# Kernel tuning notes

Hardware: AMD Instinct MI355X
Metric: run time of the kernel (lower is better)

## Reference

```python
import jax, jax.numpy as jnp
import numpy as np

N_QUBITS = 14  # matches init kwarg; state_size = 2**14 = 16384
BATCH = 4096

def setup_inputs() -> dict:
    key = jax.random.key(0)
    phi = jax.random.normal(key, (BATCH, 2 ** N_QUBITS), dtype=jnp.float32)
    return {"phi": phi}

def _fwht(x):
    """Fast Walsh-Hadamard transform, identical butterfly order to had_big:
    view as [B, 2, 2, ..., 2] and for each qubit axis i replace (a, b) with
    (a+b, a-b), then scale by 2**(-n/2)."""
    B, N = x.shape
    n = int(round(np.log2(N)))
    for i in range(n):
        # axis i of the [2]*n view == axis 2 of this reshape
        x = x.reshape(B, 2 ** i, 2, N // (2 ** (i + 1)))
        a = x[:, :, 0, :]
        b = x[:, :, 1, :]
        x = jnp.stack([a + b, a - b], axis=2)
    return x.reshape(B, N) * jnp.asarray(2.0 ** (-n / 2.0), dtype=x.dtype)

def reference(phi):
    return _fwht(phi)
```

## Files before the change

### kernel.cpp

```cpp
#include <hip/hip_runtime.h>


#define NF4 4096
#define SCALE 0.0078125f

__device__ __forceinline__ int swz(int F) { return F ^ ((F >> 3) & 7); }

__device__ __forceinline__ void bfly2(float4& a, float4& b) {
    float ax = a.x, ay = a.y, az = a.z, aw = a.w;
    float bx = b.x, by = b.y, bz = b.z, bw = b.w;
    a.x = ax + bx; a.y = ay + by; a.z = az + bz; a.w = aw + bw;
    b.x = ax - bx; b.y = ay - by; b.z = az - bz; b.w = aw - bw;
}

__device__ __forceinline__ void bfly8(float4 v[8]) {
    bfly2(v[0], v[1]); bfly2(v[2], v[3]); bfly2(v[4], v[5]); bfly2(v[6], v[7]);
    bfly2(v[0], v[2]); bfly2(v[1], v[3]); bfly2(v[4], v[6]); bfly2(v[5], v[7]);
    bfly2(v[0], v[4]); bfly2(v[1], v[5]); bfly2(v[2], v[6]); bfly2(v[3], v[7]);
}

__device__ __forceinline__ void bfly_inner(float4& t) {
    float a = t.x + t.y, b = t.x - t.y;
    float c = t.z + t.w, d = t.z - t.w;
    t.x = a + c; t.y = b + d; t.z = a - c; t.w = b - d;
}

__global__ __launch_bounds__(512)
void fwht_kernel(const float* __restrict__ in, float* __restrict__ out) {
    __shared__ float4 lds[NF4];

    const int row  = blockIdx.x;
    const int tid  = threadIdx.x;
    const int lane = tid & 63;
    const int w    = tid >> 6;

    const float4* in4  = (const float4*)in  + (size_t)row * NF4;
    float4*       out4 = (float4*)out       + (size_t)row * NF4;

    float4 v[8];

#pragma unroll
    for (int j = 0; j < 8; ++j) v[j] = in4[tid + 512 * j];
#pragma unroll
    for (int j = 0; j < 8; ++j) bfly_inner(v[j]);
    bfly8(v);

#pragma unroll
    for (int j = 0; j < 8; ++j) lds[swz(tid + 512 * j)] = v[j];
    __syncthreads();

    {
        const int base = 8 * lane + 512 * w;
#pragma unroll
        for (int g = 0; g < 8; ++g) v[g] = lds[swz(base + g)];
        bfly8(v);
#pragma unroll
        for (int g = 0; g < 8; ++g) lds[swz(base + g)] = v[g];
    }
    __syncthreads();

    {
        const int base = (tid & 7) + 64 * ((tid >> 3) & 7) + 512 * w;
#pragma unroll
        for (int g = 0; g < 8; ++g) v[g] = lds[swz(base + 8 * g)];
        bfly8(v);
#pragma unroll
        for (int g = 0; g < 8; ++g) lds[swz(base + 8 * g)] = v[g];
    }
    __syncthreads();

    {
        const int base = lane + 512 * w;
#pragma unroll
        for (int g = 0; g < 8; ++g) v[g] = lds[swz(base + 64 * g)];
        bfly8(v);
#pragma unroll
        for (int g = 0; g < 8; ++g) {
            float4 t = v[g];
            t.x *= SCALE; t.y *= SCALE; t.z *= SCALE; t.w *= SCALE;
            out4[base + 64 * g] = t;
        }
    }
}

extern "C" void kernel_launch(void* const* d_in, const int* in_sizes, int n_in,
                              void* d_out, int out_size, void* d_ws, size_t ws_size,
                              hipStream_t stream) {
    const float* phi = (const float*)d_in[0];
    float* out = (float*)d_out;
    fwht_kernel<<<4096, 512, 0, stream>>>(phi, out);
}
```

Before: 430.6 us.

## Drop intra-wave barriers, use nontemporal global I/O, simplify swizzle indexing

After the first block barrier, each wavefront works only on its own 512-element slice of LDS, so the two later __syncthreads are removed. Global loads and stores become nontemporal builtins to avoid cache pollution on the streaming read/write. The XOR swizzle is folded into precomputed per-thread offsets and the butterflies use native vector types to cut address and ALU overhead. Dropping the barriers is only correct if the 64-wide wavefront assumption and in-order LDS access within a wave hold.

```diff
diff --git a/kernel.cpp b/kernel.cpp
--- a/kernel.cpp
+++ b/kernel.cpp
@@ -4,22 +4,21 @@
 #define NF4 4096
 #define SCALE 0.0078125f
 
-__device__ __forceinline__ int swz(int F) { return F ^ ((F >> 3) & 7); }
+typedef float f4 __attribute__((ext_vector_type(4)));
 
-__device__ __forceinline__ void bfly2(float4& a, float4& b) {
-    float ax = a.x, ay = a.y, az = a.z, aw = a.w;
-    float bx = b.x, by = b.y, bz = b.z, bw = b.w;
-    a.x = ax + bx; a.y = ay + by; a.z = az + bz; a.w = aw + bw;
-    b.x = ax - bx; b.y = ay - by; b.z = az - bz; b.w = aw - bw;
+__device__ __forceinline__ void bfly2(f4& a, f4& b) {
+    f4 t = a;
+    a = t + b;
+    b = t - b;
 }
 
-__device__ __forceinline__ void bfly8(float4 v[8]) {
+__device__ __forceinline__ void bfly8(f4 v[8]) {
     bfly2(v[0], v[1]); bfly2(v[2], v[3]); bfly2(v[4], v[5]); bfly2(v[6], v[7]);
     bfly2(v[0], v[2]); bfly2(v[1], v[3]); bfly2(v[4], v[6]); bfly2(v[5], v[7]);
     bfly2(v[0], v[4]); bfly2(v[1], v[5]); bfly2(v[2], v[6]); bfly2(v[3], v[7]);
 }
 
-__device__ __forceinline__ void bfly_inner(float4& t) {
+__device__ __forceinline__ void bfly_inner(f4& t) {
     float a = t.x + t.y, b = t.x - t.y;
     float c = t.z + t.w, d = t.z - t.w;
     t.x = a + c; t.y = b + d; t.z = a - c; t.w = b - d;
@@ -27,59 +26,59 @@
 
 __global__ __launch_bounds__(512)
 void fwht_kernel(const float* __restrict__ in, float* __restrict__ out) {
-    __shared__ float4 lds[NF4];
+    __shared__ f4 lds[NF4];
 
-    const int row  = blockIdx.x;
     const int tid  = threadIdx.x;
     const int lane = tid & 63;
     const int w    = tid >> 6;
 
-    const float4* in4  = (const float4*)in  + (size_t)row * NF4;
-    float4*       out4 = (float4*)out       + (size_t)row * NF4;
+    const f4* in4  = (const f4*)in  + (size_t)blockIdx.x * NF4;
+    f4*       out4 = (f4*)out       + (size_t)blockIdx.x * NF4;
 
-    float4 v[8];
+    f4 v[8];
 
 #pragma unroll
-    for (int j = 0; j < 8; ++j) v[j] = in4[tid + 512 * j];
+    for (int j = 0; j < 8; ++j)
+        v[j] = __builtin_nontemporal_load(in4 + tid + 512 * j);
 #pragma unroll
     for (int j = 0; j < 8; ++j) bfly_inner(v[j]);
     bfly8(v);
 
+    const int st = tid ^ ((tid >> 3) & 7);
 #pragma unroll
-    for (int j = 0; j < 8; ++j) lds[swz(tid + 512 * j)] = v[j];
+    for (int j = 0; j < 8; ++j) lds[st + 512 * j] = v[j];
     __syncthreads();
 
     {
+        const int s    = lane & 7;
         const int base = 8 * lane + 512 * w;
 #pragma unroll
-        for (int g = 0; g < 8; ++g) v[g] = lds[swz(base + g)];
+        for (int g = 0; g < 8; ++g) v[g] = lds[base + (g ^ s)];
         bfly8(v);
 #pragma unroll
-        for (int g = 0; g < 8; ++g) lds[swz(base + g)] = v[g];
+        for (int g = 0; g < 8; ++g) lds[base + (g ^ s)] = v[g];
     }
-    __syncthreads();
 
     {
-        const int base = (tid & 7) + 64 * ((tid >> 3) & 7) + 512 * w;
+        const int c  = tid & 7;
+        const int b2 = 64 * ((lane >> 3) & 7) + 512 * w;
 #pragma unroll
-        for (int g = 0; g < 8; ++g) v[g] = lds[swz(base + 8 * g)];
+        for (int g = 0; g < 8; ++g) v[g] = lds[b2 + 8 * g + (c ^ g)];
         bfly8(v);
 #pragma unroll
-        for (int g = 0; g < 8; ++g) lds[swz(base + 8 * g)] = v[g];
+        for (int g = 0; g < 8; ++g) lds[b2 + 8 * g + (c ^ g)] = v[g];
     }
-    __syncthreads();
 
     {
-        const int base = lane + 512 * w;
+        const int s2 = (lane >> 3) & 7;
+        const int rb = (lane ^ s2) + 512 * w;
+        const int sb = lane + 512 * w;
 #pragma unroll
-        for (int g = 0; g < 8; ++g) v[g] = lds[swz(base + 64 * g)];
+        for (int g = 0; g < 8; ++g) v[g] = lds[rb + 64 * g];
         bfly8(v);
 #pragma unroll
-        for (int g = 0; g < 8; ++g) {
-            float4 t = v[g];
-            t.x *= SCALE; t.y *= SCALE; t.z *= SCALE; t.w *= SCALE;
-            out4[base + 64 * g] = t;
-        }
+        for (int g = 0; g < 8; ++g)
+            __builtin_nontemporal_store(v[g] * SCALE, out4 + sb + 64 * g);
     }
 }
 
```

After: 422.3 us. No clear change (-1.9%).
